# Optimization experiments

Measured on AMD Instinct MI355X. Metric: run time of the kernel, lower is better.

## Reference

```python
import jax, jax.numpy as jnp
import numpy as np


def setup_inputs() -> dict:
    key = jax.random.key(0)
    ks = jax.random.split(key, 8)
    B, C, H, W = 4, 512, 64, 64
    M = C // 8
    sq = 1.0 / np.sqrt(C)
    return {
        "x": jax.random.normal(ks[0], (B, C, H, W), jnp.float32),
        "Wq": jax.random.normal(ks[1], (M, C), jnp.float32) * sq,
        "bq": jnp.zeros((M,), jnp.float32),
        "Wk": jax.random.normal(ks[2], (M, C), jnp.float32) * sq,
        "bk": jnp.zeros((M,), jnp.float32),
        "Wv": jax.random.normal(ks[3], (C, C), jnp.float32) * sq,
        "bv": jnp.zeros((C,), jnp.float32),
        "gamma": jax.random.uniform(ks[4], (1,), jnp.float32),
    }


def reference(x, Wq, bq, Wk, bk, Wv, bv, gamma):
    B, C, H, W = x.shape
    N = H * W
    xf = x.reshape(B, C, N)  # flatten spatial -> [B, C, N]
    # 1x1 convs are channel-mixing matmuls
    q = jnp.einsum('mc,bcn->bmn', Wq, xf) + bq[None, :, None]  # [B, M, N]
    k = jnp.einsum('mc,bcn->bmn', Wk, xf) + bk[None, :, None]  # [B, M, N]
    v = jnp.einsum('dc,bcn->bdn', Wv, xf) + bv[None, :, None]  # [B, C, N]
    # sim[b,i,j] = <q[:, i], k[:, j]>, softmax over j
    sim = jnp.einsum('bmi,bmj->bij', q, k)  # [B, N, N]
    attn = jax.nn.softmax(sim, axis=-1)
    # feat[b,c,i] = sum_j v[b,c,j] * attn[b,i,j]
    feat = jnp.einsum('bcj,bij->bci', v, attn)  # [B, C, N]
    out = gamma[0] * feat.reshape(B, C, H, W) + x
    return out
```

## Files before the change

### kernel.cpp

```cpp
#include <hip/hip_runtime.h>

typedef _Float16 f16;
typedef _Float16 f16x8 __attribute__((ext_vector_type(8)));
typedef float    f32x4 __attribute__((ext_vector_type(4)));
typedef unsigned int u32x2 __attribute__((ext_vector_type(2)));

#define B_ 4
#define C_ 512
#define N_ 4096
#define M_ 64

__device__ __forceinline__ unsigned pk2(float a, float b) {
    union { f16 h[2]; unsigned u; } t;
    t.h[0] = (f16)a; t.h[1] = (f16)b;
    return t.u;
}

__global__ __launch_bounds__(256) void wcvt(
    const float* __restrict__ Wq, const float* __restrict__ Wk,
    const float* __restrict__ Wv, f16* __restrict__ Wf)
{
    const int e = (blockIdx.x * 256 + threadIdx.x) * 8;
    const float* src;
    int off;
    if (e < 32768)      { src = Wq; off = e; }
    else if (e < 65536) { src = Wk; off = e - 32768; }
    else                { src = Wv; off = e - 65536; }
    float4 a = *(const float4*)(src + off);
    float4 b = *(const float4*)(src + off + 4);
    f16x8 o;
    o[0]=(f16)a.x; o[1]=(f16)a.y; o[2]=(f16)a.z; o[3]=(f16)a.w;
    o[4]=(f16)b.x; o[5]=(f16)b.y; o[6]=(f16)b.z; o[7]=(f16)b.w;
    *(f16x8*)(Wf + e) = o;
}

__global__ __launch_bounds__(512, 2) void qkv4(
    const f16* __restrict__ Wf, const float* __restrict__ x,
    const float* __restrict__ bq, const float* __restrict__ bk,
    const float* __restrict__ bv,
    f16* __restrict__ qt, f16* __restrict__ ktf, f16* __restrict__ vf)
{
    __shared__ __align__(16) char sH[3][8192];
    __shared__ float sBias[640];

    const int tid  = threadIdx.x;
    const int w    = tid >> 6;
    const int lane = tid & 63;
    const int l15  = lane & 15;
    const int quad = lane >> 4;
    const int n0   = blockIdx.x * 64;
    const int b    = blockIdx.y;
    const int row0 = w * 80;

    for (int e = tid; e < 640; e += 512)
        sBias[e] = (e < 64) ? bq[e] : (e < 128) ? bk[e - 64] : bv[e - 128];

    const int wbyte = (lane * 128 + w * 16) ^ ((lane & 7) << 4);
    int rbyte[4][2];
    #pragma unroll
    for (int nt = 0; nt < 4; ++nt)
        #pragma unroll
        for (int kh = 0; kh < 2; ++kh)
            rbyte[nt][kh] = ((nt * 16 + l15) * 128 + kh * 64 + quad * 16)
                            ^ ((l15 & 7) << 4);

    const float* xg = x + (size_t)b * (C_ * N_) + n0 + lane;
    const f16*   wp = Wf + (size_t)row0 * 512 + quad * 8;

    float gn[2][8];
    {
        float g0[8];
        #pragma unroll
        for (int u = 0; u < 8; ++u) g0[u] = xg[(size_t)(w * 8 + u) * N_];
        #pragma unroll
        for (int u = 0; u < 8; ++u) gn[1][u] = xg[(size_t)(64 + w * 8 + u) * N_];
        f16x8 h;
        #pragma unroll
        for (int u = 0; u < 8; ++u) h[u] = (f16)g0[u];
        *(f16x8*)(&sH[0][0] + wbyte) = h;
    }
    asm volatile("s_waitcnt lgkmcnt(0)" ::: "memory");
    __builtin_amdgcn_s_barrier();
    __builtin_amdgcn_sched_barrier(0);

    f32x4 acc[5][4] = {};

    #pragma unroll
    for (int t = 0; t < 8; ++t) {
        f16x8 af[5][2];
        #pragma unroll
        for (int ot = 0; ot < 5; ++ot)
            #pragma unroll
            for (int kh = 0; kh < 2; ++kh)
                af[ot][kh] = *(const f16x8*)(wp + (size_t)(ot * 16 + l15) * 512
                                             + t * 64 + kh * 32);
        if (t + 2 < 8) {
            #pragma unroll
            for (int u = 0; u < 8; ++u)
                gn[t & 1][u] = xg[(size_t)((t + 2) * 64 + w * 8 + u) * N_];
        }
        const char* sc = &sH[t % 3][0];
        f16x8 bf[4][2];
        #pragma unroll
        for (int nt = 0; nt < 4; ++nt)
            #pragma unroll
            for (int kh = 0; kh < 2; ++kh)
                bf[nt][kh] = *(const f16x8*)(sc + rbyte[nt][kh]);

        #pragma unroll
        for (int ot = 0; ot < 5; ++ot)
            #pragma unroll
            for (int kh = 0; kh < 2; ++kh)
                #pragma unroll
                for (int nt = 0; nt < 4; ++nt)
                    acc[ot][nt] = __builtin_amdgcn_mfma_f32_16x16x32_f16(
                        af[ot][kh], bf[nt][kh], acc[ot][nt], 0, 0, 0);

        if (t + 1 < 8) {
            f16x8 h;
            #pragma unroll
            for (int u = 0; u < 8; ++u) h[u] = (f16)gn[(t + 1) & 1][u];
            *(f16x8*)(&sH[(t + 1) % 3][0] + wbyte) = h;
        }
        asm volatile("s_waitcnt lgkmcnt(0)" ::: "memory");
        __builtin_amdgcn_s_barrier();
        __builtin_amdgcn_sched_barrier(0);
    }

    #pragma unroll
    for (int ot = 0; ot < 5; ++ot) {
        const int rowBase = row0 + ot * 16;
        const int rq = rowBase + quad * 4;
        #pragma unroll
        for (int nt = 0; nt < 4; ++nt) {
            const int n = n0 + nt * 16 + l15;
            union { f16 h[4]; unsigned long long u; } pkv;
            #pragma unroll
            for (int r = 0; r < 4; ++r)
                pkv.h[r] = (f16)(acc[ot][nt][r] + sBias[rq + r]);
            if (rowBase < 64) {
                *(unsigned long long*)(qt + ((size_t)(b * N_ + n)) * M_ + rq) = pkv.u;
            } else if (rowBase < 128) {
                const int ol = rq - 64;
                size_t idx = (((size_t)b * 256 + (n >> 4)) * 2 + (ol >> 5)) * 512
                           + (size_t)((((ol >> 3) & 3) * 16 + (n & 15)) * 8) + (ol & 7);
                *(unsigned long long*)(ktf + idx) = pkv.u;
            } else {
                const int c = rq - 128;
                #pragma unroll
                for (int r = 0; r < 4; ++r) {
                    size_t idx = ((size_t)b * (C_ * N_)) + (size_t)((c + r) >> 4) * 65536
                               + (size_t)(n >> 6) * 1024 + (size_t)((n >> 5) & 1) * 512
                               + (size_t)((((n >> 3) & 3) * 16 + ((c + r) & 15)) * 8) + (n & 7);
                    vf[idx] = pkv.h[r];
                }
            }
        }
    }
}

__global__ __launch_bounds__(512, 2) void attn(
    const f16* __restrict__ qt, const f16* __restrict__ ktf,
    const f16* __restrict__ vf, const float* __restrict__ x,
    const float* __restrict__ gamma, float* __restrict__ out)
{
    __shared__ __align__(16) char Pb[2][8192];
    __shared__ float mxs[8][4][16];
    __shared__ float lss[8][4][16];

    const int tid  = threadIdx.x;
    const int w    = tid >> 6;
    const int lane = tid & 63;
    const int l15  = lane & 15;
    const int quad = lane >> 4;
    const int jt   = w & 3;
    const int ish  = w >> 2;
    const int is0  = ish * 2, is1 = is0 + 1;

    const int lin  = blockIdx.x;
    const int b    = (lin & 7) >> 1;
    const int iblk = ((lin >> 3) << 1) | (lin & 1);
    const int i0   = iblk * 64;

    const f16* kln = ktf + (size_t)b * (N_ * M_) + lane * 8;
    const f16* vln = vf  + (size_t)b * (C_ * N_) + lane * 8;

    f16x8 bqf[4][2];
    #pragma unroll
    for (int is = 0; is < 4; ++is)
        #pragma unroll
        for (int kh = 0; kh < 2; ++kh)
            bqf[is][kh] = *(const f16x8*)(qt + ((size_t)(b * N_ + i0 + is * 16 + l15)) * M_
                                          + kh * 32 + quad * 8);

    float mx[4];
    #pragma unroll
    for (int is = 0; is < 4; ++is) mx[is] = -3.0e38f;
    {
        const f16* kw = kln + (size_t)(w * 512) * 64;
        f16x8 akc[4][2];
        #pragma unroll
        for (int t = 0; t < 4; ++t)
            #pragma unroll
            for (int kh = 0; kh < 2; ++kh)
                akc[t][kh] = *(const f16x8*)(kw + t * 1024 + kh * 512);

        #pragma unroll 2
        for (int jj = 0; jj < 512; jj += 64) {
            f16x8 akn[4][2];
            if (jj + 64 < 512) {
                const f16* kn = kw + (size_t)(jj + 64) * 64;
                #pragma unroll
                for (int t = 0; t < 4; ++t)
                    #pragma unroll
                    for (int kh = 0; kh < 2; ++kh)
                        akn[t][kh] = *(const f16x8*)(kn + t * 1024 + kh * 512);
            }
            #pragma unroll
            for (int t = 0; t < 4; ++t) {
                #pragma unroll
                for (int is = 0; is < 4; ++is) {
                    f32x4 s = {};
                    s = __builtin_amdgcn_mfma_f32_16x16x32_f16(akc[t][0], bqf[is][0], s, 0, 0, 0);
                    s = __builtin_amdgcn_mfma_f32_16x16x32_f16(akc[t][1], bqf[is][1], s, 0, 0, 0);
                    mx[is] = fmaxf(mx[is], fmaxf(fmaxf(s[0], s[1]), fmaxf(s[2], s[3])));
                }
            }
            #pragma unroll
            for (int t = 0; t < 4; ++t)
                #pragma unroll
                for (int kh = 0; kh < 2; ++kh)
                    akc[t][kh] = akn[t][kh];
        }
    }
    #pragma unroll
    for (int is = 0; is < 4; ++is) {
        mx[is] = fmaxf(mx[is], __shfl_xor(mx[is], 16, 64));
        mx[is] = fmaxf(mx[is], __shfl_xor(mx[is], 32, 64));
    }
    if (lane < 16) {
        #pragma unroll
        for (int is = 0; is < 4; ++is) mxs[w][is][lane] = mx[is];
    }
    __syncthreads();
    float m0 = -3.0e38f, m1 = -3.0e38f;
    #pragma unroll
    for (int w2 = 0; w2 < 8; ++w2) {
        m0 = fmaxf(m0, mxs[w2][is0][l15]);
        m1 = fmaxf(m1, mxs[w2][is1][l15]);
    }

    f32x4 acc[4][4] = {};
    float lp0 = 0.f, lp1 = 0.f;

    char* pbB = (char*)&Pb[0][0];
    const int swz = (l15 & 7) << 4;
    const int wb0 = ((is0 * 16 + l15) * 128 + (jt * 16 + quad * 4) * 2) ^ swz;
    const int wb1 = wb0 + 2048;
    int rb[4][2];
    #pragma unroll
    for (int is = 0; is < 4; ++is)
        #pragma unroll
        for (int kh = 0; kh < 2; ++kh)
            rb[is][kh] = ((is * 16 + l15) * 128 + kh * 64 + quad * 16) ^ swz;

    const f16* kp = kln + (size_t)(jt * 16) * 64;
    const int cw = w * 4;

    f16x8 akr[2][2];
    f16x8 vr[2][8];

    akr[0][0] = *(const f16x8*)(kp);
    akr[0][1] = *(const f16x8*)(kp + 512);
    {
        f32x4 s0 = {}, s1 = {};
        s0 = __builtin_amdgcn_mfma_f32_16x16x32_f16(akr[0][0], bqf[is0][0], s0, 0, 0, 0);
        s0 = __builtin_amdgcn_mfma_f32_16x16x32_f16(akr[0][1], bqf[is0][1], s0, 0, 0, 0);
        s1 = __builtin_amdgcn_mfma_f32_16x16x32_f16(akr[0][0], bqf[is1][0], s1, 0, 0, 0);
        s1 = __builtin_amdgcn_mfma_f32_16x16x32_f16(akr[0][1], bqf[is1][1], s1, 0, 0, 0);
        float p0 = __expf(s0[0] - m0), p1 = __expf(s0[1] - m0);
        float p2 = __expf(s0[2] - m0), p3 = __expf(s0[3] - m0);
        lp0 += (p0 + p1) + (p2 + p3);
        u32x2 pw0 = { pk2(p0, p1), pk2(p2, p3) };
        *(u32x2*)(pbB + wb0) = pw0;
        float q0 = __expf(s1[0] - m1), q1 = __expf(s1[1] - m1);
        float q2 = __expf(s1[2] - m1), q3 = __expf(s1[3] - m1);
        lp1 += (q0 + q1) + (q2 + q3);
        u32x2 pw1 = { pk2(q0, q1), pk2(q2, q3) };
        *(u32x2*)(pbB + wb1) = pw1;
    }
    akr[1][0] = *(const f16x8*)(kp + 4096);
    akr[1][1] = *(const f16x8*)(kp + 4096 + 512);
    #pragma unroll
    for (int ct = 0; ct < 4; ++ct) {
        vr[0][ct]     = *(const f16x8*)(vln + (size_t)(cw + ct) * 65536);
        vr[0][ct + 4] = *(const f16x8*)(vln + (size_t)(cw + ct) * 65536 + 512);
    }
    __syncthreads();

#define ATTN_BODY(T, CBc, NBc) {                                              \
    f16x8 pbf[4][2];                                                          \
    _Pragma("unroll")                                                         \
    for (int is_ = 0; is_ < 4; ++is_)                                         \
        _Pragma("unroll")                                                     \
        for (int kh_ = 0; kh_ < 2; ++kh_)                                     \
            pbf[is_][kh_] = *(const f16x8*)(pbB + (CBc) * 8192 + rb[is_][kh_]); \
    f32x4 s0 = {}, s1 = {};                                                   \
    s0 = __builtin_amdgcn_mfma_f32_16x16x32_f16(akr[NBc][0], bqf[is0][0], s0, 0, 0, 0); \
    s0 = __builtin_amdgcn_mfma_f32_16x16x32_f16(akr[NBc][1], bqf[is0][1], s0, 0, 0, 0); \
    s1 = __builtin_amdgcn_mfma_f32_16x16x32_f16(akr[NBc][0], bqf[is1][0], s1, 0, 0, 0); \
    s1 = __builtin_amdgcn_mfma_f32_16x16x32_f16(akr[NBc][1], bqf[is1][1], s1, 0, 0, 0); \
    if ((T) + 2 < 64) {                                                       \
        const f16* kn_ = kp + (size_t)((T) + 2) * 4096;                       \
        akr[CBc][0] = *(const f16x8*)(kn_);                                   \
        akr[CBc][1] = *(const f16x8*)(kn_ + 512);                             \
    }                                                                         \
    {                                                                         \
        const f16* vt_ = vln + (size_t)((T) + 1) * 1024;                      \
        _Pragma("unroll")                                                     \
        for (int ct_ = 0; ct_ < 4; ++ct_) {                                   \
            vr[NBc][ct_]     = *(const f16x8*)(vt_ + (size_t)(cw + ct_) * 65536);       \
            vr[NBc][ct_ + 4] = *(const f16x8*)(vt_ + (size_t)(cw + ct_) * 65536 + 512); \
        }                                                                     \
    }                                                                         \
    {                                                                         \
        float p0 = __expf(s0[0] - m0), p1 = __expf(s0[1] - m0);               \
        float p2 = __expf(s0[2] - m0), p3 = __expf(s0[3] - m0);               \
        lp0 += (p0 + p1) + (p2 + p3);                                         \
        u32x2 pw = { pk2(p0, p1), pk2(p2, p3) };                              \
        *(u32x2*)(pbB + (NBc) * 8192 + wb0) = pw;                             \
    }                                                                         \
    {                                                                         \
        float q0 = __expf(s1[0] - m1), q1 = __expf(s1[1] - m1);               \
        float q2 = __expf(s1[2] - m1), q3 = __expf(s1[3] - m1);               \
        lp1 += (q0 + q1) + (q2 + q3);                                         \
        u32x2 pw = { pk2(q0, q1), pk2(q2, q3) };                              \
        *(u32x2*)(pbB + (NBc) * 8192 + wb1) = pw;                             \
    }                                                                         \
    __builtin_amdgcn_s_setprio(1);                                            \
    _Pragma("unroll")                                                         \
    for (int ct_ = 0; ct_ < 4; ++ct_)                                         \
        _Pragma("unroll")                                                     \
        for (int is_ = 0; is_ < 4; ++is_)                                     \
            acc[ct_][is_] = __builtin_amdgcn_mfma_f32_16x16x32_f16(           \
                vr[CBc][ct_], pbf[is_][0], acc[ct_][is_], 0, 0, 0);           \
    _Pragma("unroll")                                                         \
    for (int ct_ = 0; ct_ < 4; ++ct_)                                         \
        _Pragma("unroll")                                                     \
        for (int is_ = 0; is_ < 4; ++is_)                                     \
            acc[ct_][is_] = __builtin_amdgcn_mfma_f32_16x16x32_f16(           \
                vr[CBc][ct_ + 4], pbf[is_][1], acc[ct_][is_], 0, 0, 0);       \
    __builtin_amdgcn_s_setprio(0);                                            \
    asm volatile("s_waitcnt lgkmcnt(0)" ::: "memory");                        \
    __builtin_amdgcn_s_barrier();                                             \
    __builtin_amdgcn_sched_barrier(0);                                        \
}

    for (int tt = 0; tt < 62; tt += 2) {
        ATTN_BODY(tt,     0, 1);
        ATTN_BODY(tt + 1, 1, 0);
    }
    ATTN_BODY(62, 0, 1);

    {
        f16x8 pbf[4][2];
        #pragma unroll
        for (int is = 0; is < 4; ++is)
            #pragma unroll
            for (int kh = 0; kh < 2; ++kh)
                pbf[is][kh] = *(const f16x8*)(pbB + 8192 + rb[is][kh]);
        #pragma unroll
        for (int ct = 0; ct < 4; ++ct)
            #pragma unroll
            for (int is = 0; is < 4; ++is)
                acc[ct][is] = __builtin_amdgcn_mfma_f32_16x16x32_f16(vr[1][ct], pbf[is][0], acc[ct][is], 0, 0, 0);
        #pragma unroll
        for (int ct = 0; ct < 4; ++ct)
            #pragma unroll
            for (int is = 0; is < 4; ++is)
                acc[ct][is] = __builtin_amdgcn_mfma_f32_16x16x32_f16(vr[1][ct + 4], pbf[is][1], acc[ct][is], 0, 0, 0);
    }

    lp0 += __shfl_xor(lp0, 16, 64);
    lp0 += __shfl_xor(lp0, 32, 64);
    lp1 += __shfl_xor(lp1, 16, 64);
    lp1 += __shfl_xor(lp1, 32, 64);
    if (lane < 16) { lss[w][is0][lane] = lp0; lss[w][is1][lane] = lp1; }
    __syncthreads();

    float linv[4];
    #pragma unroll
    for (int is = 0; is < 4; ++is) {
        const int wb = (is >> 1) * 4;
        float l = (lss[wb + 0][is][l15] + lss[wb + 1][is][l15])
                + (lss[wb + 2][is][l15] + lss[wb + 3][is][l15]);
        linv[is] = 1.0f / l;
    }

    const float g = gamma[0];
    #pragma unroll
    for (int is = 0; is < 4; ++is) {
        const int i = i0 + is * 16 + l15;
        #pragma unroll
        for (int ct = 0; ct < 4; ++ct) {
            #pragma unroll
            for (int r = 0; r < 4; ++r) {
                const int c = w * 64 + ct * 16 + quad * 4 + r;
                const size_t idx = ((size_t)(b * C_ + c)) * N_ + i;
                out[idx] = g * (acc[ct][is][r] * linv[is]) + x[idx];
            }
        }
    }
}

extern "C" void kernel_launch(void* const* d_in, const int* in_sizes, int n_in,
                              void* d_out, int out_size, void* d_ws, size_t ws_size,
                              hipStream_t stream)
{
    const float* x     = (const float*)d_in[0];
    const float* Wq    = (const float*)d_in[1];
    const float* bq    = (const float*)d_in[2];
    const float* Wk    = (const float*)d_in[3];
    const float* bk    = (const float*)d_in[4];
    const float* Wv    = (const float*)d_in[5];
    const float* bv    = (const float*)d_in[6];
    const float* gamma = (const float*)d_in[7];
    float* out = (float*)d_out;

    char* ws = (char*)d_ws;
    f16* qt  = (f16*)ws;
    f16* ktf = qt + (size_t)B_ * N_ * M_;
    f16* vf  = ktf + (size_t)B_ * N_ * M_;
    f16* Wf  = vf + (size_t)B_ * C_ * N_;

    wcvt<<<dim3(160), 256, 0, stream>>>(Wq, Wk, Wv, Wf);
    qkv4<<<dim3(N_ / 64, B_), 512, 0, stream>>>(Wf, x, bq, bk, bv, qt, ktf, vf);
    attn<<<dim3(256), 512, 0, stream>>>(qt, ktf, vf, x, gamma, out);
}
```

Baseline: 219.9 us.

## Fuse QKV projection and attention into one cooperative kernel with grid sync

Merges the QKV projection kernel and the attention kernel into a single cooperative launch of 256 blocks. A grid-wide sync separates the two phases, and both phases share one shared-memory buffer. This removes a kernel launch and the gap between the two kernels. In exchange it adds a grid barrier and a cooperative-launch requirement, and the projection phase now runs as 256 blocks with a different block-to-(n, b) mapping.

```diff
diff --git a/kernel.cpp b/kernel.cpp
--- a/kernel.cpp
+++ b/kernel.cpp
@@ -1,4 +1,7 @@
 #include <hip/hip_runtime.h>
+#include <hip/hip_cooperative_groups.h>
+
+namespace cg = cooperative_groups;
 
 typedef _Float16 f16;
 typedef _Float16 f16x8 __attribute__((ext_vector_type(8)));
@@ -33,270 +36,6 @@
     o[4]=(f16)b.x; o[5]=(f16)b.y; o[6]=(f16)b.z; o[7]=(f16)b.w;
     *(f16x8*)(Wf + e) = o;
 }
-
-__global__ __launch_bounds__(512, 2) void qkv4(
-    const f16* __restrict__ Wf, const float* __restrict__ x,
-    const float* __restrict__ bq, const float* __restrict__ bk,
-    const float* __restrict__ bv,
-    f16* __restrict__ qt, f16* __restrict__ ktf, f16* __restrict__ vf)
-{
-    __shared__ __align__(16) char sH[3][8192];
-    __shared__ float sBias[640];
-
-    const int tid  = threadIdx.x;
-    const int w    = tid >> 6;
-    const int lane = tid & 63;
-    const int l15  = lane & 15;
-    const int quad = lane >> 4;
-    const int n0   = blockIdx.x * 64;
-    const int b    = blockIdx.y;
-    const int row0 = w * 80;
-
-    for (int e = tid; e < 640; e += 512)
-        sBias[e] = (e < 64) ? bq[e] : (e < 128) ? bk[e - 64] : bv[e - 128];
-
-    const int wbyte = (lane * 128 + w * 16) ^ ((lane & 7) << 4);
-    int rbyte[4][2];
-    #pragma unroll
-    for (int nt = 0; nt < 4; ++nt)
-        #pragma unroll
-        for (int kh = 0; kh < 2; ++kh)
-            rbyte[nt][kh] = ((nt * 16 + l15) * 128 + kh * 64 + quad * 16)
-                            ^ ((l15 & 7) << 4);
-
-    const float* xg = x + (size_t)b * (C_ * N_) + n0 + lane;
-    const f16*   wp = Wf + (size_t)row0 * 512 + quad * 8;
-
-    float gn[2][8];
-    {
-        float g0[8];
-        #pragma unroll
-        for (int u = 0; u < 8; ++u) g0[u] = xg[(size_t)(w * 8 + u) * N_];
-        #pragma unroll
-        for (int u = 0; u < 8; ++u) gn[1][u] = xg[(size_t)(64 + w * 8 + u) * N_];
-        f16x8 h;
-        #pragma unroll
-        for (int u = 0; u < 8; ++u) h[u] = (f16)g0[u];
-        *(f16x8*)(&sH[0][0] + wbyte) = h;
-    }
-    asm volatile("s_waitcnt lgkmcnt(0)" ::: "memory");
-    __builtin_amdgcn_s_barrier();
-    __builtin_amdgcn_sched_barrier(0);
-
-    f32x4 acc[5][4] = {};
-
-    #pragma unroll
-    for (int t = 0; t < 8; ++t) {
-        f16x8 af[5][2];
-        #pragma unroll
-        for (int ot = 0; ot < 5; ++ot)
-            #pragma unroll
-            for (int kh = 0; kh < 2; ++kh)
-                af[ot][kh] = *(const f16x8*)(wp + (size_t)(ot * 16 + l15) * 512
-                                             + t * 64 + kh * 32);
-        if (t + 2 < 8) {
-            #pragma unroll
-            for (int u = 0; u < 8; ++u)
-                gn[t & 1][u] = xg[(size_t)((t + 2) * 64 + w * 8 + u) * N_];
-        }
-        const char* sc = &sH[t % 3][0];
-        f16x8 bf[4][2];
-        #pragma unroll
-        for (int nt = 0; nt < 4; ++nt)
-            #pragma unroll
-            for (int kh = 0; kh < 2; ++kh)
-                bf[nt][kh] = *(const f16x8*)(sc + rbyte[nt][kh]);
-
-        #pragma unroll
-        for (int ot = 0; ot < 5; ++ot)
-            #pragma unroll
-            for (int kh = 0; kh < 2; ++kh)
-                #pragma unroll
-                for (int nt = 0; nt < 4; ++nt)
-                    acc[ot][nt] = __builtin_amdgcn_mfma_f32_16x16x32_f16(
-                        af[ot][kh], bf[nt][kh], acc[ot][nt], 0, 0, 0);
-
-        if (t + 1 < 8) {
-            f16x8 h;
-            #pragma unroll
-            for (int u = 0; u < 8; ++u) h[u] = (f16)gn[(t + 1) & 1][u];
-            *(f16x8*)(&sH[(t + 1) % 3][0] + wbyte) = h;
-        }
-        asm volatile("s_waitcnt lgkmcnt(0)" ::: "memory");
-        __builtin_amdgcn_s_barrier();
-        __builtin_amdgcn_sched_barrier(0);
-    }
-
-    #pragma unroll
-    for (int ot = 0; ot < 5; ++ot) {
-        const int rowBase = row0 + ot * 16;
-        const int rq = rowBase + quad * 4;
-        #pragma unroll
-        for (int nt = 0; nt < 4; ++nt) {
-            const int n = n0 + nt * 16 + l15;
-            union { f16 h[4]; unsigned long long u; } pkv;
-            #pragma unroll
-            for (int r = 0; r < 4; ++r)
-                pkv.h[r] = (f16)(acc[ot][nt][r] + sBias[rq + r]);
-            if (rowBase < 64) {
-                *(unsigned long long*)(qt + ((size_t)(b * N_ + n)) * M_ + rq) = pkv.u;
-            } else if (rowBase < 128) {
-                const int ol = rq - 64;
-                size_t idx = (((size_t)b * 256 + (n >> 4)) * 2 + (ol >> 5)) * 512
-                           + (size_t)((((ol >> 3) & 3) * 16 + (n & 15)) * 8) + (ol & 7);
-                *(unsigned long long*)(ktf + idx) = pkv.u;
-            } else {
-                const int c = rq - 128;
-                #pragma unroll
-                for (int r = 0; r < 4; ++r) {
-                    size_t idx = ((size_t)b * (C_ * N_)) + (size_t)((c + r) >> 4) * 65536
-                               + (size_t)(n >> 6) * 1024 + (size_t)((n >> 5) & 1) * 512
-                               + (size_t)((((n >> 3) & 3) * 16 + ((c + r) & 15)) * 8) + (n & 7);
-                    vf[idx] = pkv.h[r];
-                }
-            }
-        }
-    }
-}
-
-__global__ __launch_bounds__(512, 2) void attn(
-    const f16* __restrict__ qt, const f16* __restrict__ ktf,
-    const f16* __restrict__ vf, const float* __restrict__ x,
-    const float* __restrict__ gamma, float* __restrict__ out)
-{
-    __shared__ __align__(16) char Pb[2][8192];
-    __shared__ float mxs[8][4][16];
-    __shared__ float lss[8][4][16];
-
-    const int tid  = threadIdx.x;
-    const int w    = tid >> 6;
-    const int lane = tid & 63;
-    const int l15  = lane & 15;
-    const int quad = lane >> 4;
-    const int jt   = w & 3;
-    const int ish  = w >> 2;
-    const int is0  = ish * 2, is1 = is0 + 1;
-
-    const int lin  = blockIdx.x;
-    const int b    = (lin & 7) >> 1;
-    const int iblk = ((lin >> 3) << 1) | (lin & 1);
-    const int i0   = iblk * 64;
-
-    const f16* kln = ktf + (size_t)b * (N_ * M_) + lane * 8;
-    const f16* vln = vf  + (size_t)b * (C_ * N_) + lane * 8;
-
-    f16x8 bqf[4][2];
-    #pragma unroll
-    for (int is = 0; is < 4; ++is)
-        #pragma unroll
-        for (int kh = 0; kh < 2; ++kh)
-            bqf[is][kh] = *(const f16x8*)(qt + ((size_t)(b * N_ + i0 + is * 16 + l15)) * M_
-                                          + kh * 32 + quad * 8);
-
-    float mx[4];
-    #pragma unroll
-    for (int is = 0; is < 4; ++is) mx[is] = -3.0e38f;
-    {
-        const f16* kw = kln + (size_t)(w * 512) * 64;
-        f16x8 akc[4][2];
-        #pragma unroll
-        for (int t = 0; t < 4; ++t)
-            #pragma unroll
-            for (int kh = 0; kh < 2; ++kh)
-                akc[t][kh] = *(const f16x8*)(kw + t * 1024 + kh * 512);
-
-        #pragma unroll 2
-        for (int jj = 0; jj < 512; jj += 64) {
-            f16x8 akn[4][2];
-            if (jj + 64 < 512) {
-                const f16* kn = kw + (size_t)(jj + 64) * 64;
-                #pragma unroll
-                for (int t = 0; t < 4; ++t)
-                    #pragma unroll
-                    for (int kh = 0; kh < 2; ++kh)
-                        akn[t][kh] = *(const f16x8*)(kn + t * 1024 + kh * 512);
-            }
-            #pragma unroll
-            for (int t = 0; t < 4; ++t) {
-                #pragma unroll
-                for (int is = 0; is < 4; ++is) {
-                    f32x4 s = {};
-                    s = __builtin_amdgcn_mfma_f32_16x16x32_f16(akc[t][0], bqf[is][0], s, 0, 0, 0);
-                    s = __builtin_amdgcn_mfma_f32_16x16x32_f16(akc[t][1], bqf[is][1], s, 0, 0, 0);
-                    mx[is] = fmaxf(mx[is], fmaxf(fmaxf(s[0], s[1]), fmaxf(s[2], s[3])));
-                }
-            }
-            #pragma unroll
-            for (int t = 0; t < 4; ++t)
-                #pragma unroll
-                for (int kh = 0; kh < 2; ++kh)
-                    akc[t][kh] = akn[t][kh];
-        }
-    }
-    #pragma unroll
-    for (int is = 0; is < 4; ++is) {
-        mx[is] = fmaxf(mx[is], __shfl_xor(mx[is], 16, 64));
-        mx[is] = fmaxf(mx[is], __shfl_xor(mx[is], 32, 64));
-    }
-    if (lane < 16) {
-        #pragma unroll
-        for (int is = 0; is < 4; ++is) mxs[w][is][lane] = mx[is];
-    }
-    __syncthreads();
-    float m0 = -3.0e38f, m1 = -3.0e38f;
-    #pragma unroll
-    for (int w2 = 0; w2 < 8; ++w2) {
-        m0 = fmaxf(m0, mxs[w2][is0][l15]);
-        m1 = fmaxf(m1, mxs[w2][is1][l15]);
-    }
-
-    f32x4 acc[4][4] = {};
-    float lp0 = 0.f, lp1 = 0.f;
-
-    char* pbB = (char*)&Pb[0][0];
-    const int swz = (l15 & 7) << 4;
-    const int wb0 = ((is0 * 16 + l15) * 128 + (jt * 16 + quad * 4) * 2) ^ swz;
-    const int wb1 = wb0 + 2048;
-    int rb[4][2];
-    #pragma unroll
-    for (int is = 0; is < 4; ++is)
-        #pragma unroll
-        for (int kh = 0; kh < 2; ++kh)
-            rb[is][kh] = ((is * 16 + l15) * 128 + kh * 64 + quad * 16) ^ swz;
-
-    const f16* kp = kln + (size_t)(jt * 16) * 64;
-    const int cw = w * 4;
-
-    f16x8 akr[2][2];
-    f16x8 vr[2][8];
-
-    akr[0][0] = *(const f16x8*)(kp);
-    akr[0][1] = *(const f16x8*)(kp + 512);
-    {
-        f32x4 s0 = {}, s1 = {};
-        s0 = __builtin_amdgcn_mfma_f32_16x16x32_f16(akr[0][0], bqf[is0][0], s0, 0, 0, 0);
-        s0 = __builtin_amdgcn_mfma_f32_16x16x32_f16(akr[0][1], bqf[is0][1], s0, 0, 0, 0);
-        s1 = __builtin_amdgcn_mfma_f32_16x16x32_f16(akr[0][0], bqf[is1][0], s1, 0, 0, 0);
-        s1 = __builtin_amdgcn_mfma_f32_16x16x32_f16(akr[0][1], bqf[is1][1], s1, 0, 0, 0);
-        float p0 = __expf(s0[0] - m0), p1 = __expf(s0[1] - m0);
-        float p2 = __expf(s0[2] - m0), p3 = __expf(s0[3] - m0);
-        lp0 += (p0 + p1) + (p2 + p3);
-        u32x2 pw0 = { pk2(p0, p1), pk2(p2, p3) };
-        *(u32x2*)(pbB + wb0) = pw0;
-        float q0 = __expf(s1[0] - m1), q1 = __expf(s1[1] - m1);
-        float q2 = __expf(s1[2] - m1), q3 = __expf(s1[3] - m1);
-        lp1 += (q0 + q1) + (q2 + q3);
-        u32x2 pw1 = { pk2(q0, q1), pk2(q2, q3) };
-        *(u32x2*)(pbB + wb1) = pw1;
-    }
-    akr[1][0] = *(const f16x8*)(kp + 4096);
-    akr[1][1] = *(const f16x8*)(kp + 4096 + 512);
-    #pragma unroll
-    for (int ct = 0; ct < 4; ++ct) {
-        vr[0][ct]     = *(const f16x8*)(vln + (size_t)(cw + ct) * 65536);
-        vr[0][ct + 4] = *(const f16x8*)(vln + (size_t)(cw + ct) * 65536 + 512);
-    }
-    __syncthreads();
 
 #define ATTN_BODY(T, CBc, NBc) {                                              \
     f16x8 pbf[4][2];                                                          \
@@ -356,58 +95,318 @@
     __builtin_amdgcn_sched_barrier(0);                                        \
 }
 
-    for (int tt = 0; tt < 62; tt += 2) {
-        ATTN_BODY(tt,     0, 1);
-        ATTN_BODY(tt + 1, 1, 0);
+__global__ __launch_bounds__(512, 2) void fused(
+    const f16* __restrict__ Wf, const float* __restrict__ x,
+    const float* __restrict__ bq, const float* __restrict__ bk,
+    const float* __restrict__ bv, const float* __restrict__ gamma,
+    f16* __restrict__ qt, f16* __restrict__ ktf, f16* __restrict__ vf,
+    float* __restrict__ out)
+{
+    __shared__ __align__(16) char smem[27648];
+    const int tid  = threadIdx.x;
+    const int w    = tid >> 6;
+    const int lane = tid & 63;
+    const int l15  = lane & 15;
+    const int quad = lane >> 4;
+    const int lin  = blockIdx.x;
+
+    {
+        const int n0   = (lin >> 2) * 64;
+        const int b    = lin & 3;
+        const int row0 = w * 80;
+        char*  sH    = smem;
+        float* sBias = (float*)(smem + 24576);
+
+        for (int e = tid; e < 640; e += 512)
+            sBias[e] = (e < 64) ? bq[e] : (e < 128) ? bk[e - 64] : bv[e - 128];
+
+        const int wbyte = (lane * 128 + w * 16) ^ ((lane & 7) << 4);
+        int rbyte[4][2];
+        #pragma unroll
+        for (int nt = 0; nt < 4; ++nt)
+            #pragma unroll
+            for (int kh = 0; kh < 2; ++kh)
+                rbyte[nt][kh] = ((nt * 16 + l15) * 128 + kh * 64 + quad * 16)
+                                ^ ((l15 & 7) << 4);
+
+        const float* xg = x + (size_t)b * (C_ * N_) + n0 + lane;
+        const f16*   wp = Wf + (size_t)row0 * 512 + quad * 8;
+
+        float gn[2][8];
+        {
+            float g0[8];
+            #pragma unroll
+            for (int u = 0; u < 8; ++u) g0[u] = xg[(size_t)(w * 8 + u) * N_];
+            #pragma unroll
+            for (int u = 0; u < 8; ++u) gn[1][u] = xg[(size_t)(64 + w * 8 + u) * N_];
+            f16x8 h;
+            #pragma unroll
+            for (int u = 0; u < 8; ++u) h[u] = (f16)g0[u];
+            *(f16x8*)(sH + wbyte) = h;
+        }
+        asm volatile("s_waitcnt lgkmcnt(0)" ::: "memory");
+        __builtin_amdgcn_s_barrier();
+        __builtin_amdgcn_sched_barrier(0);
+
+        f32x4 acc[5][4] = {};
+
+        #pragma unroll
+        for (int t = 0; t < 8; ++t) {
+            f16x8 af[5][2];
+            #pragma unroll
+            for (int ot = 0; ot < 5; ++ot)
+                #pragma unroll
+                for (int kh = 0; kh < 2; ++kh)
+                    af[ot][kh] = *(const f16x8*)(wp + (size_t)(ot * 16 + l15) * 512
+                                                 + t * 64 + kh * 32);
+            if (t + 2 < 8) {
+                #pragma unroll
+                for (int u = 0; u < 8; ++u)
+                    gn[t & 1][u] = xg[(size_t)((t + 2) * 64 + w * 8 + u) * N_];
+            }
+            const char* sc = sH + (t % 3) * 8192;
+            f16x8 bf[4][2];
+            #pragma unroll
+            for (int nt = 0; nt < 4; ++nt)
+                #pragma unroll
+                for (int kh = 0; kh < 2; ++kh)
+                    bf[nt][kh] = *(const f16x8*)(sc + rbyte[nt][kh]);
+
+            #pragma unroll
+            for (int ot = 0; ot < 5; ++ot)
+                #pragma unroll
+                for (int kh = 0; kh < 2; ++kh)
+                    #pragma unroll
+                    for (int nt = 0; nt < 4; ++nt)
+                        acc[ot][nt] = __builtin_amdgcn_mfma_f32_16x16x32_f16(
+                            af[ot][kh], bf[nt][kh], acc[ot][nt], 0, 0, 0);
+
+            if (t + 1 < 8) {
+                f16x8 h;
+                #pragma unroll
+                for (int u = 0; u < 8; ++u) h[u] = (f16)gn[(t + 1) & 1][u];
+                *(f16x8*)(sH + ((t + 1) % 3) * 8192 + wbyte) = h;
+            }
+            asm volatile("s_waitcnt lgkmcnt(0)" ::: "memory");
+            __builtin_amdgcn_s_barrier();
+            __builtin_amdgcn_sched_barrier(0);
+        }
+
+        #pragma unroll
+        for (int ot = 0; ot < 5; ++ot) {
+            const int rowBase = row0 + ot * 16;
+            const int rq = rowBase + quad * 4;
+            #pragma unroll
+            for (int nt = 0; nt < 4; ++nt) {
+                const int n = n0 + nt * 16 + l15;
+                union { f16 h[4]; unsigned long long u; } pkv;
+                #pragma unroll
+                for (int r = 0; r < 4; ++r)
+                    pkv.h[r] = (f16)(acc[ot][nt][r] + sBias[rq + r]);
+                if (rowBase < 64) {
+                    *(unsigned long long*)(qt + ((size_t)(b * N_ + n)) * M_ + rq) = pkv.u;
+                } else if (rowBase < 128) {
+                    const int ol = rq - 64;
+                    size_t idx = (((size_t)b * 256 + (n >> 4)) * 2 + (ol >> 5)) * 512
+                               + (size_t)((((ol >> 3) & 3) * 16 + (n & 15)) * 8) + (ol & 7);
+                    *(unsigned long long*)(ktf + idx) = pkv.u;
+                } else {
+                    const int c = rq - 128;
+                    #pragma unroll
+                    for (int r = 0; r < 4; ++r) {
+                        size_t idx = ((size_t)b * (C_ * N_)) + (size_t)((c + r) >> 4) * 65536
+                                   + (size_t)(n >> 6) * 1024 + (size_t)((n >> 5) & 1) * 512
+                                   + (size_t)((((n >> 3) & 3) * 16 + ((c + r) & 15)) * 8) + (n & 7);
+                        vf[idx] = pkv.h[r];
+                    }
+                }
+            }
+        }
     }
-    ATTN_BODY(62, 0, 1);
+
+    cg::this_grid().sync();
 
     {
-        f16x8 pbf[4][2];
+        char* pbB = smem;
+        float (*mxs)[4][16] = (float (*)[4][16])(smem + 16384);
+        float (*lss)[4][16] = (float (*)[4][16])(smem + 18432);
+
+        const int jt   = w & 3;
+        const int ish  = w >> 2;
+        const int is0  = ish * 2, is1 = is0 + 1;
+
+        const int b    = (lin & 7) >> 1;
+        const int iblk = ((lin >> 3) << 1) | (lin & 1);
+        const int i0   = iblk * 64;
+
+        const f16* kln = ktf + (size_t)b * (N_ * M_) + lane * 8;
+        const f16* vln = vf  + (size_t)b * (C_ * N_) + lane * 8;
+
+        f16x8 bqf[4][2];
         #pragma unroll
         for (int is = 0; is < 4; ++is)
             #pragma unroll
             for (int kh = 0; kh < 2; ++kh)
-                pbf[is][kh] = *(const f16x8*)(pbB + 8192 + rb[is][kh]);
-        #pragma unroll
-        for (int ct = 0; ct < 4; ++ct)
+                bqf[is][kh] = *(const f16x8*)(qt + ((size_t)(b * N_ + i0 + is * 16 + l15)) * M_
+                                              + kh * 32 + quad * 8);
+
+        float mx[4];
+        #pragma unroll
+        for (int is = 0; is < 4; ++is) mx[is] = -3.0e38f;
+        {
+            const f16* kw = kln + (size_t)(w * 512) * 64;
+            f16x8 akc[4][2];
+            #pragma unroll
+            for (int t = 0; t < 4; ++t)
+                #pragma unroll
+                for (int kh = 0; kh < 2; ++kh)
+                    akc[t][kh] = *(const f16x8*)(kw + t * 1024 + kh * 512);
+
+            #pragma unroll 2
+            for (int jj = 0; jj < 512; jj += 64) {
+                f16x8 akn[4][2];
+                if (jj + 64 < 512) {
+                    const f16* kn = kw + (size_t)(jj + 64) * 64;
+                    #pragma unroll
+                    for (int t = 0; t < 4; ++t)
+                        #pragma unroll
+                        for (int kh = 0; kh < 2; ++kh)
+                            akn[t][kh] = *(const f16x8*)(kn + t * 1024 + kh * 512);
+                }
+                #pragma unroll
+                for (int t = 0; t < 4; ++t) {
+                    #pragma unroll
+                    for (int is = 0; is < 4; ++is) {
+                        f32x4 s = {};
+                        s = __builtin_amdgcn_mfma_f32_16x16x32_f16(akc[t][0], bqf[is][0], s, 0, 0, 0);
+                        s = __builtin_amdgcn_mfma_f32_16x16x32_f16(akc[t][1], bqf[is][1], s, 0, 0, 0);
+                        mx[is] = fmaxf(mx[is], fmaxf(fmaxf(s[0], s[1]), fmaxf(s[2], s[3])));
+                    }
+                }
+                #pragma unroll
+                for (int t = 0; t < 4; ++t)
+                    #pragma unroll
+                    for (int kh = 0; kh < 2; ++kh)
+                        akc[t][kh] = akn[t][kh];
+            }
+        }
+        #pragma unroll
+        for (int is = 0; is < 4; ++is) {
+            mx[is] = fmaxf(mx[is], __shfl_xor(mx[is], 16, 64));
+            mx[is] = fmaxf(mx[is], __shfl_xor(mx[is], 32, 64));
+        }
+        if (lane < 16) {
+            #pragma unroll
+            for (int is = 0; is < 4; ++is) mxs[w][is][lane] = mx[is];
+        }
+        __syncthreads();
+        float m0 = -3.0e38f, m1 = -3.0e38f;
+        #pragma unroll
+        for (int w2 = 0; w2 < 8; ++w2) {
+            m0 = fmaxf(m0, mxs[w2][is0][l15]);
+            m1 = fmaxf(m1, mxs[w2][is1][l15]);
+        }
+
+        f32x4 acc[4][4] = {};
+        float lp0 = 0.f, lp1 = 0.f;
+
+        const int swz = (l15 & 7) << 4;
+        const int wb0 = ((is0 * 16 + l15) * 128 + (jt * 16 + quad * 4) * 2) ^ swz;
+        const int wb1 = wb0 + 2048;
+        int rb[4][2];
+        #pragma unroll
+        for (int is = 0; is < 4; ++is)
+            #pragma unroll
+            for (int kh = 0; kh < 2; ++kh)
+                rb[is][kh] = ((is * 16 + l15) * 128 + kh * 64 + quad * 16) ^ swz;
+
+        const f16* kp = kln + (size_t)(jt * 16) * 64;
+        const int cw = w * 4;
+
+        f16x8 akr[2][2];
+        f16x8 vr[2][8];
+
+        akr[0][0] = *(const f16x8*)(kp);
+        akr[0][1] = *(const f16x8*)(kp + 512);
+        {
+            f32x4 s0 = {}, s1 = {};
+            s0 = __builtin_amdgcn_mfma_f32_16x16x32_f16(akr[0][0], bqf[is0][0], s0, 0, 0, 0);
+            s0 = __builtin_amdgcn_mfma_f32_16x16x32_f16(akr[0][1], bqf[is0][1], s0, 0, 0, 0);
+            s1 = __builtin_amdgcn_mfma_f32_16x16x32_f16(akr[0][0], bqf[is1][0], s1, 0, 0, 0);
+            s1 = __builtin_amdgcn_mfma_f32_16x16x32_f16(akr[0][1], bqf[is1][1], s1, 0, 0, 0);
+            float p0 = __expf(s0[0] - m0), p1 = __expf(s0[1] - m0);
+            float p2 = __expf(s0[2] - m0), p3 = __expf(s0[3] - m0);
+            lp0 += (p0 + p1) + (p2 + p3);
+            u32x2 pw0 = { pk2(p0, p1), pk2(p2, p3) };
+            *(u32x2*)(pbB + wb0) = pw0;
+            float q0 = __expf(s1[0] - m1), q1 = __expf(s1[1] - m1);
+            float q2 = __expf(s1[2] - m1), q3 = __expf(s1[3] - m1);
+            lp1 += (q0 + q1) + (q2 + q3);
+            u32x2 pw1 = { pk2(q0, q1), pk2(q2, q3) };
+            *(u32x2*)(pbB + wb1) = pw1;
+        }
+        akr[1][0] = *(const f16x8*)(kp + 4096);
+        akr[1][1] = *(const f16x8*)(kp + 4096 + 512);
+        #pragma unroll
+        for (int ct = 0; ct < 4; ++ct) {
+            vr[0][ct]     = *(const f16x8*)(vln + (size_t)(cw + ct) * 65536);
+            vr[0][ct + 4] = *(const f16x8*)(vln + (size_t)(cw + ct) * 65536 + 512);
+        }
+        __syncthreads();
+
+        for (int tt = 0; tt < 62; tt += 2) {
+            ATTN_BODY(tt,     0, 1);
+            ATTN_BODY(tt + 1, 1, 0);
+        }
+        ATTN_BODY(62, 0, 1);
+
+        {
+            f16x8 pbf[4][2];
             #pragma unroll
             for (int is = 0; is < 4; ++is)
-                acc[ct][is] = __builtin_amdgcn_mfma_f32_16x16x32_f16(vr[1][ct], pbf[is][0], acc[ct][is], 0, 0, 0);
-        #pragma unroll
-        for (int ct = 0; ct < 4; ++ct)
-            #pragma unroll
-            for (int is = 0; is < 4; ++is)
-                acc[ct][is] = __builtin_amdgcn_mfma_f32_16x16x32_f16(vr[1][ct + 4], pbf[is][1], acc[ct][is], 0, 0, 0);
-    }
-
-    lp0 += __shfl_xor(lp0, 16, 64);
-    lp0 += __shfl_xor(lp0, 32, 64);
-    lp1 += __shfl_xor(lp1, 16, 64);
-    lp1 += __shfl_xor(lp1, 32, 64);
-    if (lane < 16) { lss[w][is0][lane] = lp0; lss[w][is1][lane] = lp1; }
-    __syncthreads();
-
-    float linv[4];
-    #pragma unroll
-    for (int is = 0; is < 4; ++is) {
-        const int wb = (is >> 1) * 4;
-        float l = (lss[wb + 0][is][l15] + lss[wb + 1][is][l15])
-                + (lss[wb + 2][is][l15] + lss[wb + 3][is][l15]);
-        linv[is] = 1.0f / l;
-    }
-
-    const float g = gamma[0];
-    #pragma unroll
-    for (int is = 0; is < 4; ++is) {
-        const int i = i0 + is * 16 + l15;
-        #pragma unroll
-        for (int ct = 0; ct < 4; ++ct) {
-            #pragma unroll
-            for (int r = 0; r < 4; ++r) {
-                const int c = w * 64 + ct * 16 + quad * 4 + r;
-                const size_t idx = ((size_t)(b * C_ + c)) * N_ + i;
-                out[idx] = g * (acc[ct][is][r] * linv[is]) + x[idx];
+                #pragma unroll
+                for (int kh = 0; kh < 2; ++kh)
+                    pbf[is][kh] = *(const f16x8*)(pbB + 8192 + rb[is][kh]);
+            #pragma unroll
+            for (int ct = 0; ct < 4; ++ct)
+                #pragma unroll
+                for (int is = 0; is < 4; ++is)
+                    acc[ct][is] = __builtin_amdgcn_mfma_f32_16x16x32_f16(vr[1][ct], pbf[is][0], acc[ct][is], 0, 0, 0);
+            #pragma unroll
+            for (int ct = 0; ct < 4; ++ct)
+                #pragma unroll
+                for (int is = 0; is < 4; ++is)
+                    acc[ct][is] = __builtin_amdgcn_mfma_f32_16x16x32_f16(vr[1][ct + 4], pbf[is][1], acc[ct][is], 0, 0, 0);
+        }
+
+        lp0 += __shfl_xor(lp0, 16, 64);
+        lp0 += __shfl_xor(lp0, 32, 64);
+        lp1 += __shfl_xor(lp1, 16, 64);
+        lp1 += __shfl_xor(lp1, 32, 64);
+        if (lane < 16) { lss[w][is0][lane] = lp0; lss[w][is1][lane] = lp1; }
+        __syncthreads();
+
+        float linv[4];
+        #pragma unroll
+        for (int is = 0; is < 4; ++is) {
+            const int wb = (is >> 1) * 4;
+            float l = (lss[wb + 0][is][l15] + lss[wb + 1][is][l15])
+                    + (lss[wb + 2][is][l15] + lss[wb + 3][is][l15]);
+            linv[is] = 1.0f / l;
+        }
+
+        const float g = gamma[0];
+        #pragma unroll
+        for (int is = 0; is < 4; ++is) {
+            const int i = i0 + is * 16 + l15;
+            #pragma unroll
+            for (int ct = 0; ct < 4; ++ct) {
+                #pragma unroll
+                for (int r = 0; r < 4; ++r) {
+                    const int c = w * 64 + ct * 16 + quad * 4 + r;
+                    const size_t idx = ((size_t)(b * C_ + c)) * N_ + i;
+                    out[idx] = g * (acc[ct][is][r] * linv[is]) + x[idx];
+                }
             }
         }
     }
@@ -434,6 +433,9 @@
     f16* Wf  = vf + (size_t)B_ * C_ * N_;
 
     wcvt<<<dim3(160), 256, 0, stream>>>(Wq, Wk, Wv, Wf);
-    qkv4<<<dim3(N_ / 64, B_), 512, 0, stream>>>(Wf, x, bq, bk, bv, qt, ktf, vf);
-    attn<<<dim3(256), 512, 0, stream>>>(qt, ktf, vf, x, gamma, out);
+
+    const f16* WfC = Wf;
+    void* args[] = { (void*)&WfC, (void*)&x, (void*)&bq, (void*)&bk, (void*)&bv,
+                     (void*)&gamma, (void*)&qt, (void*)&ktf, (void*)&vf, (void*)&out };
+    hipLaunchCooperativeKernel((void*)fused, dim3(256), dim3(512), args, 0, stream);
 }
```

After: 282.0 us. 1.28x slower.
